# Optimization experiments

Hardware: AMD Instinct MI355X
Metric: run time of the kernel (lower is better)

The kernel has to match this reference:

```python
import jax, jax.numpy as jnp
import numpy as np

B, T, D, NH = 2, 2048, 2048, 16
HID = D  # hidden_dim must equal emb_dim for the source's fc2(x1) to type-check
HD = D // NH
EPS = 1e-5


def setup_inputs() -> dict:
    key = jax.random.key(0)
    ks = jax.random.split(key, 16)
    s = 0.02
    inp = {
        "x": jax.random.normal(ks[0], (B, T, D), jnp.float32),
        "Wq": jax.random.normal(ks[1], (D, D), jnp.float32) * s,
        "bq": jnp.zeros((D,), jnp.float32),
        "Wk": jax.random.normal(ks[2], (D, D), jnp.float32) * s,
        "bk": jnp.zeros((D,), jnp.float32),
        "Wv": jax.random.normal(ks[3], (D, D), jnp.float32) * s,
        "bv": jnp.zeros((D,), jnp.float32),
        "Wo": jax.random.normal(ks[4], (D, D), jnp.float32) * s,
        "bo": jnp.zeros((D,), jnp.float32),
        "scale1": jnp.ones((D,), jnp.float32),
        "scale2": jnp.ones((D,), jnp.float32),
        "W1": jax.random.normal(ks[5], (D, HID), jnp.float32) * s,
        "W2": jax.random.normal(ks[6], (D, HID), jnp.float32) * s,  # fc2: Linear(emb_dim, hidden_dim)
        "W3": jax.random.normal(ks[7], (HID, D), jnp.float32) * s,
    }
    return inp


def _rmsnorm(x, scale):
    m = jnp.mean(x * x, axis=-1, keepdims=True)
    return scale * (x * jax.lax.rsqrt(m + EPS))


def _attention(x, Wq, bq, Wk, bk, Wv, bv, Wo, bo):
    b, t, _ = x.shape
    q = (x @ Wq + bq).reshape(b, t, NH, HD)
    k = (x @ Wk + bk).reshape(b, t, NH, HD)
    v = (x @ Wv + bv).reshape(b, t, NH, HD)
    # energy: [B, H, T, T]; softmax over keys, scaled by 1/sqrt(head_dim); NO causal mask in source
    energy = jnp.einsum("bqhd,bkhd->bhqk", q, k) / jnp.sqrt(jnp.float32(HD))
    attn = jax.nn.softmax(energy, axis=-1)
    out = jnp.einsum("bhqk,bkhd->bqhd", attn, v).reshape(b, t, D)
    return out @ Wo + bo


def _ffn(x, W1, W2, W3):
    x1 = x @ W1                       # [B,T,HID]
    x2 = x1 @ W2                      # source quirk: fc2 applied to x1 (hidden_dim == emb_dim)
    return (x1 * jax.nn.sigmoid(x1) * x2) @ W3


def reference(x, Wq, bq, Wk, bk, Wv, bv, Wo, bo, scale1, scale2, W1, W2, W3):
    shortcut = x
    h = _rmsnorm(x, scale1)
    h = _attention(h, Wq, bq, Wk, bk, Wv, bv, Wo, bo)
    h = shortcut + h
    h = _rmsnorm(h, scale2)
    h = _ffn(h, W1, W2, W3)
    # source adds the ORIGINAL input again (shortcut never reassigned)
    return h + shortcut
```

## Files before the change

kernel.cpp:

```cpp
#include <hip/hip_runtime.h>

typedef __bf16 bf16x8 __attribute__((ext_vector_type(8)));
typedef __bf16 bf16x4v __attribute__((ext_vector_type(4)));
typedef float  f32x4  __attribute__((ext_vector_type(4)));

#define LDS_AS(p) ((__attribute__((address_space(3))) void*)(p))
#define GLB_AS(p) ((const __attribute__((address_space(1))) void*)(p))

#define QSCL (0.08838834764831845f * 1.4426950408889634f)

struct TP { const float* s[7]; __bf16* d[7]; float sc[7]; };
__global__ __launch_bounds__(256) void transpose_convert_all(TP p) {
  const float* __restrict__ W = p.s[blockIdx.z];
  __bf16* __restrict__ Wt = p.d[blockIdx.z];
  const float sc = p.sc[blockIdx.z];
  __shared__ float tile[32][33];
  const int tx = threadIdx.x & 31, ty = threadIdx.x >> 5;
  const int n0 = blockIdx.x * 32, k0 = blockIdx.y * 32;
#pragma unroll
  for (int j = 0; j < 4; ++j)
    tile[ty + j * 8][tx] = W[(size_t)(k0 + ty + j * 8) * 2048 + n0 + tx];
  __syncthreads();
#pragma unroll
  for (int j = 0; j < 4; ++j)
    Wt[(size_t)(n0 + ty + j * 8) * 2048 + k0 + tx] = (__bf16)(tile[tx][ty + j * 8] * sc);
}

__global__ __launch_bounds__(256) void rmsnorm_k(
    const float* __restrict__ x, const float* __restrict__ scale,
    __bf16* __restrict__ out) {
  const int row = blockIdx.x, t = threadIdx.x;
  const float4* xr = (const float4*)(x + (size_t)row * 2048);
  float4 a = xr[t], b2 = xr[t + 256];
  float ss = a.x * a.x + a.y * a.y + a.z * a.z + a.w * a.w +
             b2.x * b2.x + b2.y * b2.y + b2.z * b2.z + b2.w * b2.w;
#pragma unroll
  for (int ofs = 32; ofs; ofs >>= 1) ss += __shfl_xor(ss, ofs, 64);
  __shared__ float red[4];
  if ((t & 63) == 0) red[t >> 6] = ss;
  __syncthreads();
  ss = red[0] + red[1] + red[2] + red[3];
  const float rs = rsqrtf(ss * (1.f / 2048.f) + 1e-5f);
  const float4* sr = (const float4*)scale;
  float4 s1 = sr[t], s2 = sr[t + 256];
  __bf16* orow = out + (size_t)row * 2048;
  orow[t * 4 + 0] = (__bf16)(a.x * rs * s1.x);
  orow[t * 4 + 1] = (__bf16)(a.y * rs * s1.y);
  orow[t * 4 + 2] = (__bf16)(a.z * rs * s1.z);
  orow[t * 4 + 3] = (__bf16)(a.w * rs * s1.w);
  orow[(t + 256) * 4 + 0] = (__bf16)(b2.x * rs * s2.x);
  orow[(t + 256) * 4 + 1] = (__bf16)(b2.y * rs * s2.y);
  orow[(t + 256) * 4 + 2] = (__bf16)(b2.z * rs * s2.z);
  orow[(t + 256) * 4 + 3] = (__bf16)(b2.w * rs * s2.w);
}

template <bool OUTF32, bool HASBIAS, bool HASRES, bool SILU, bool VTRANS>
__global__ __launch_bounds__(512, 2) void gemm_bt2(
    const __bf16* __restrict__ A, const __bf16* __restrict__ Bt,
    const float* __restrict__ bias, const float* __restrict__ res,
    const __bf16* __restrict__ ew, void* __restrict__ Cout,
    int M, int N, int Kd) {
  __shared__ __attribute__((aligned(16))) char lds[2][3][16384];

  const int tid = threadIdx.x;
  const int w = tid >> 6, l = tid & 63;
  const int wr = w >> 1, wc = w & 1;
  const int lm = l & 15, lq = l >> 4;

  const int flat = blockIdx.y * 16 + blockIdx.x;
  const int swz = (flat & 7) * 32 + (flat >> 3);
  const int bx = swz >> 4, by = swz & 15;
  const int N0 = bx * 128, M0 = by * 256;

  const int srow = w * 8 + (l >> 3);
  const int scol = ((l & 7) ^ (l >> 3)) * 8;
  const __bf16* aS = A + (size_t)(M0 + srow) * Kd + scol;
  const __bf16* bS = Bt + (size_t)(N0 + srow) * Kd + scol;

  auto stageHT = [&](int t, int s, int db) {
    char* dst = lds[db][s] + w * 1024;
    const __bf16* src = (s == 0) ? (bS + t * 64)
                                 : (aS + (size_t)(s - 1) * 128 * Kd + t * 64);
    __builtin_amdgcn_global_load_lds(GLB_AS(src), LDS_AS(dst), 16, 0, 0);
    __builtin_amdgcn_global_load_lds(GLB_AS(src + (size_t)64 * Kd), LDS_AS(dst + 8192), 16, 0, 0);
  };

  f32x4 acc[4][4];
#pragma unroll
  for (int m = 0; m < 4; ++m)
#pragma unroll
    for (int n = 0; n < 4; ++n)
#pragma unroll
      for (int e = 0; e < 4; ++e) acc[m][n][e] = 0.f;

  const int swzr = (lm & 7) << 4;
  const int c0 = (lq * 16) ^ swzr;
  const int c1 = ((64 + lq * 16)) ^ swzr;
  const int arow = (wr & 1) * 8192 + lm * 128;
  const int brow = wc * 8192 + lm * 128;

  stageHT(0, 0, 0); stageHT(0, 1, 0); stageHT(0, 2, 0);
  stageHT(1, 0, 1); stageHT(1, 1, 1);
  asm volatile("s_waitcnt vmcnt(4)" ::: "memory");
  __builtin_amdgcn_s_barrier();

  const int NT = Kd >> 6;
  bf16x8 af[4][2], bfr[4][2];

#define BAR()                                            \
  do {                                                   \
    asm volatile("" ::: "memory");                       \
    __builtin_amdgcn_s_barrier();                        \
    asm volatile("" ::: "memory");                       \
  } while (0)

#define MFMA_QUAD(MB, NB)                                                          \
  do {                                                                             \
    _Pragma("unroll") for (int m = 0; m < 2; ++m)                                  \
      _Pragma("unroll") for (int n = 0; n < 2; ++n) {                              \
        acc[(MB) + m][(NB) + n] = __builtin_amdgcn_mfma_f32_16x16x32_bf16(         \
            af[(MB) + m][0], bfr[(NB) + n][0], acc[(MB) + m][(NB) + n], 0, 0, 0);  \
        acc[(MB) + m][(NB) + n] = __builtin_amdgcn_mfma_f32_16x16x32_bf16(         \
            af[(MB) + m][1], bfr[(NB) + n][1], acc[(MB) + m][(NB) + n], 0, 0, 0);  \
      }                                                                            \
  } while (0)

#define TILE_BODY(T, BUF)                                                       \
  do {                                                                          \
    const char* Ab = lds[BUF][1 + (wr >> 1)];                                   \
    const char* Bb = lds[BUF][0];                                               \
         \
    _Pragma("unroll") for (int m = 0; m < 4; ++m) {                             \
      af[m][0] = *(const bf16x8*)(Ab + arow + m * 2048 + c0);                   \
      af[m][1] = *(const bf16x8*)(Ab + arow + m * 2048 + c1);                   \
    }                                                                           \
    _Pragma("unroll") for (int n = 0; n < 4; ++n) {                             \
      bfr[n][0] = *(const bf16x8*)(Bb + brow + n * 2048 + c0);                  \
      bfr[n][1] = *(const bf16x8*)(Bb + brow + n * 2048 + c1);                  \
    }                                                                           \
    if ((T) + 1 < NT) stageHT((T) + 1, 2, (BUF) ^ 1);                           \
    BAR();                                                                      \
    __builtin_amdgcn_s_setprio(1);                                              \
    MFMA_QUAD(0, 0);                                                            \
    __builtin_amdgcn_s_setprio(0);                                              \
    asm volatile("s_waitcnt lgkmcnt(0)" ::: "memory");                          \
    BAR();                                                                      \
                                          \
    if ((T) + 2 < NT) stageHT((T) + 2, 0, BUF);                                 \
    BAR();                                                                      \
    __builtin_amdgcn_s_setprio(1);                                              \
    MFMA_QUAD(0, 2);                                                            \
    __builtin_amdgcn_s_setprio(0);                                              \
    BAR();                                                                      \
                                          \
    if ((T) + 2 < NT) stageHT((T) + 2, 1, BUF);                                 \
    BAR();                                                                      \
    __builtin_amdgcn_s_setprio(1);                                              \
    MFMA_QUAD(2, 0);                                                            \
    __builtin_amdgcn_s_setprio(0);                                              \
    BAR();                                                                      \
                                             \
    __builtin_amdgcn_s_setprio(1);                                              \
    MFMA_QUAD(2, 2);                                                            \
    __builtin_amdgcn_s_setprio(0);                                              \
    if ((T) + 2 < NT) { asm volatile("s_waitcnt vmcnt(4)" ::: "memory"); }      \
    else { asm volatile("s_waitcnt vmcnt(0)" ::: "memory"); }                   \
    BAR();                                                                      \
  } while (0)

  for (int tp = 0; tp < NT; tp += 2) {
    TILE_BODY(tp, 0);
    TILE_BODY(tp + 1, 1);
  }
#undef TILE_BODY
#undef MFMA_QUAD
#undef BAR

#pragma unroll
  for (int mt = 0; mt < 4; ++mt) {
#pragma unroll
    for (int nt = 0; nt < 4; ++nt) {
      const int col = N0 + wc * 64 + nt * 16 + lm;
      float bv = 0.f;
      if (HASBIAS) bv = bias[col];
      if (VTRANS) {
        const int rw0 = M0 + wr * 64 + mt * 16 + lq * 4;
        const int bidx = rw0 >> 11, tok = rw0 & 2047;
        bf16x4v pk;
#pragma unroll
        for (int i = 0; i < 4; ++i) pk[i] = (__bf16)(acc[mt][nt][i] + bv);
        *(bf16x4v*)((__bf16*)Cout + ((size_t)(bidx * 2048 + col)) * 2048 + tok) = pk;
      } else {
#pragma unroll
        for (int i = 0; i < 4; ++i) {
          const int row = M0 + wr * 64 + mt * 16 + lq * 4 + i;
          const size_t off = (size_t)row * N + col;
          float v = acc[mt][nt][i] + bv;
          if (HASRES) v += res[off];
          if (SILU) {
            const float x1v = (float)ew[off];
            v = x1v * (1.f / (1.f + __expf(-x1v))) * v;
          }
          if (OUTF32) ((float*)Cout)[off] = v;
          else ((__bf16*)Cout)[off] = (__bf16)v;
        }
      }
    }
  }
}

__global__ __launch_bounds__(512, 2) void gemm_qkv(
    const __bf16* __restrict__ A, const __bf16* __restrict__ Bt,
    const float* __restrict__ bq, const float* __restrict__ bk,
    __bf16* __restrict__ Qout, __bf16* __restrict__ Kout, int Kd) {
  __shared__ __attribute__((aligned(16))) char lds[2][4][16384];

  const int tid = threadIdx.x;
  const int w = tid >> 6, l = tid & 63;
  const int wr = w >> 2, wc = w & 3;
  const int lm = l & 15, lq = l >> 4;

  const int flat = blockIdx.y * 16 + blockIdx.x;
  const int swz = (flat & 7) * 32 + (flat >> 3);
  const int bx = swz >> 4, by = swz & 15;
  const int N0 = bx * 256, M0 = by * 256;

  const int srow = w * 8 + (l >> 3);
  const int scol = ((l & 7) ^ (l >> 3)) * 8;
  const __bf16* aS = A + (size_t)(M0 + srow) * Kd + scol;
  const __bf16* bS = Bt + (size_t)(N0 + srow) * Kd + scol;

  auto stageHT = [&](int t, int s, int db) {
    char* dst = lds[db][s] + w * 1024;
    const __bf16* src = (s >= 2) ? (aS + (size_t)(s - 2) * 128 * Kd + t * 64)
                                 : (bS + (size_t)s * 128 * Kd + t * 64);
    __builtin_amdgcn_global_load_lds(GLB_AS(src), LDS_AS(dst), 16, 0, 0);
    __builtin_amdgcn_global_load_lds(GLB_AS(src + (size_t)64 * Kd), LDS_AS(dst + 8192), 16, 0, 0);
  };

  f32x4 acc[8][4];
#pragma unroll
  for (int m = 0; m < 8; ++m)
#pragma unroll
    for (int n = 0; n < 4; ++n)
#pragma unroll
      for (int e = 0; e < 4; ++e) acc[m][n][e] = 0.f;

  const int swzr = (lm & 7) << 4;
  const int c0 = (lq * 16) ^ swzr;
  const int c1 = ((64 + lq * 16)) ^ swzr;
  const int arow = lm * 128;
  const int brow = ((wc & 1) * 64 + lm) * 128;

  stageHT(0, 0, 0); stageHT(0, 1, 0); stageHT(0, 2, 0); stageHT(0, 3, 0);
  stageHT(1, 0, 1); stageHT(1, 1, 1); stageHT(1, 2, 1);
  asm volatile("s_waitcnt vmcnt(6)" ::: "memory");
  __builtin_amdgcn_s_barrier();

  const int NT = Kd >> 6;
  bf16x8 af[4][2], bfr[4][2];

#define BAR()                                            \
  do {                                                   \
    asm volatile("" ::: "memory");                       \
    __builtin_amdgcn_s_barrier();                        \
    asm volatile("" ::: "memory");                       \
  } while (0)

#define MFMA_QUAD(MB, NB)                                                          \
  do {                                                                             \
    _Pragma("unroll") for (int m = 0; m < 4; ++m)                                  \
      _Pragma("unroll") for (int n = 0; n < 2; ++n) {                              \
        acc[(MB) + m][(NB) + n] = __builtin_amdgcn_mfma_f32_16x16x32_bf16(         \
            af[m][0], bfr[(NB) + n][0], acc[(MB) + m][(NB) + n], 0, 0, 0);         \
        acc[(MB) + m][(NB) + n] = __builtin_amdgcn_mfma_f32_16x16x32_bf16(         \
            af[m][1], bfr[(NB) + n][1], acc[(MB) + m][(NB) + n], 0, 0, 0);         \
      }                                                                            \
  } while (0)

#define TILE_BODY(T, BUF)                                                       \
  do {                                                                          \
    const char* Ab = lds[BUF][2 + wr];                                          \
    const char* Bb = lds[BUF][wc >> 1];                                         \
    _Pragma("unroll") for (int m = 0; m < 4; ++m) {                             \
      af[m][0] = *(const bf16x8*)(Ab + arow + m * 2048 + c0);                   \
      af[m][1] = *(const bf16x8*)(Ab + arow + m * 2048 + c1);                   \
    }                                                                           \
    _Pragma("unroll") for (int n = 0; n < 4; ++n) {                             \
      bfr[n][0] = *(const bf16x8*)(Bb + brow + n * 2048 + c0);                  \
      bfr[n][1] = *(const bf16x8*)(Bb + brow + n * 2048 + c1);                  \
    }                                                                           \
    if ((T) + 1 < NT) stageHT((T) + 1, 3, (BUF) ^ 1);                           \
    BAR();                                                                      \
    __builtin_amdgcn_s_setprio(1);                                              \
    MFMA_QUAD(0, 0);                                                            \
    __builtin_amdgcn_s_setprio(0);                                              \
    asm volatile("s_waitcnt lgkmcnt(0)" ::: "memory");                          \
    BAR();                                                                      \
    if ((T) + 2 < NT) stageHT((T) + 2, 0, BUF);                                 \
    BAR();                                                                      \
    __builtin_amdgcn_s_setprio(1);                                              \
    MFMA_QUAD(0, 2);                                                            \
    __builtin_amdgcn_s_setprio(0);                                              \
    BAR();                                                                      \
    _Pragma("unroll") for (int m = 0; m < 4; ++m) {                             \
      af[m][0] = *(const bf16x8*)(Ab + arow + (m + 4) * 2048 + c0);             \
      af[m][1] = *(const bf16x8*)(Ab + arow + (m + 4) * 2048 + c1);             \
    }                                                                           \
    if ((T) + 2 < NT) stageHT((T) + 2, 1, BUF);                                 \
    BAR();                                                                      \
    __builtin_amdgcn_s_setprio(1);                                              \
    MFMA_QUAD(4, 0);                                                            \
    __builtin_amdgcn_s_setprio(0);                                              \
    asm volatile("s_waitcnt lgkmcnt(0)" ::: "memory");                          \
    BAR();                                                                      \
    if ((T) + 2 < NT) stageHT((T) + 2, 2, BUF);                                 \
    BAR();                                                                      \
    __builtin_amdgcn_s_setprio(1);                                              \
    MFMA_QUAD(4, 2);                                                            \
    __builtin_amdgcn_s_setprio(0);                                              \
    if ((T) + 2 < NT) { asm volatile("s_waitcnt vmcnt(6)" ::: "memory"); }      \
    else { asm volatile("s_waitcnt vmcnt(0)" ::: "memory"); }                   \
    BAR();                                                                      \
  } while (0)

  for (int tp = 0; tp < NT; tp += 2) {
    TILE_BODY(tp, 0);
    TILE_BODY(tp + 1, 1);
  }
#undef TILE_BODY
#undef MFMA_QUAD
#undef BAR

  const int seg = N0 >> 11;
  const int nbase = N0 & 2047;
  const float* bb = (seg == 0) ? bq : bk;
  const float bsc = (seg == 0) ? QSCL : 1.f;
  __bf16* dst = (seg == 0) ? Qout : Kout;
#pragma unroll
  for (int m = 0; m < 8; ++m) {
#pragma unroll
    for (int n = 0; n < 4; ++n) {
      const int col = nbase + wc * 64 + n * 16 + lm;
      const float bvv = bb[col] * bsc;
#pragma unroll
      for (int i = 0; i < 4; ++i) {
        const int row = M0 + wr * 128 + m * 16 + lq * 4 + i;
        dst[(size_t)row * 2048 + col] = (__bf16)(acc[m][n][i] + bvv);
      }
    }
  }
}

__global__ __launch_bounds__(256, 2) void attn_mfma(
    const __bf16* __restrict__ Q, const __bf16* __restrict__ K,
    const __bf16* __restrict__ Vt, __bf16* __restrict__ O) {
  __shared__ __attribute__((aligned(16))) char KsL[2][16 * 1024];
  __shared__ __attribute__((aligned(16))) char VsL[2][16 * 1024];

  const int t = threadIdx.x;
  const int w = t >> 6, l = t & 63;
  const int lm = l & 15, quad = l >> 4;
  const int flat = (blockIdx.z * gridDim.y + blockIdx.y) * gridDim.x + blockIdx.x;
  const int swz = (flat & 7) * 64 + (flat >> 3);
  const int b = swz >> 8;
  const int h = (swz >> 4) & 15;
  const int q0 = (swz & 15) * 128;
  const size_t Ds = 2048;
  const size_t hoff = (size_t)h * 128;
  const size_t bbase = (size_t)b * 2048;
  const int slq = (lm << 2) | quad;
  const int sl16 = (slq ^ ((slq >> 3) & 7)) * 16;

  const int slog = l ^ ((l >> 3) & 7);
  const int krow = slog >> 2, kcol = (slog & 3) * 8;
  const int vth = l & 3, vd = l >> 2;

  bf16x8 onesv;
#pragma unroll
  for (int i = 0; i < 8; ++i) onesv[i] = (__bf16)1.0f;

  bf16x8 qf[2][4];
#pragma unroll
  for (int ntq = 0; ntq < 2; ++ntq)
#pragma unroll
    for (int ks = 0; ks < 4; ++ks)
      qf[ntq][ks] = *(const bf16x8*)(Q + (bbase + q0 + w * 32 + ntq * 16 + lm) * Ds + hoff + ks * 32 + quad * 8);

  f32x4 oacc[2][8];
#pragma unroll
  for (int ntq = 0; ntq < 2; ++ntq)
#pragma unroll
    for (int nv = 0; nv < 8; ++nv)
#pragma unroll
      for (int e = 0; e < 4; ++e) oacc[ntq][nv][e] = 0.f;
  f32x4 lacc[2];
#pragma unroll
  for (int ntq = 0; ntq < 2; ++ntq)
#pragma unroll
    for (int e = 0; e < 4; ++e) lacc[ntq][e] = 0.f;

  bf16x8 vreg[4];

  auto loadV = [&](int kt) {
#pragma unroll
    for (int i = 0; i < 4; ++i) {
      const int chunk = w * 4 + i;
      const int nv = chunk >> 1, c = chunk & 1;
      vreg[i] = *(const bf16x8*)(Vt + (bbase + hoff + nv * 16 + vd) * Ds + kt + c * 32 + vth * 8);
    }
  };
  auto stageK = [&](int kt, char* Kb) {
#pragma unroll
    for (int i = 0; i < 4; ++i) {
      const __bf16* src = K + (bbase + kt + i * 16 + krow) * Ds + hoff + w * 32 + kcol;
      __builtin_amdgcn_global_load_lds(GLB_AS(src), LDS_AS(Kb + (i * 4 + w) * 1024), 16, 0, 0);
    }
  };
  auto writeV = [&](char* Vb) {
    const int slot_a = (vd << 2) | ((vth & 1) << 1);
    const int o_a = (slot_a ^ ((vd >> 1) & 7)) * 16 + (vth >> 1) * 8;
#pragma unroll
    for (int i = 0; i < 4; ++i) {
      char* base = Vb + (w * 4 + i) * 1024;
      uint4 u = *(const uint4*)&vreg[i];
      *(uint2*)(base + o_a) = make_uint2(u.x, u.y);
      *(uint2*)(base + (o_a ^ 16)) = make_uint2(u.z, u.w);
    }
  };

  loadV(0);
  stageK(0, KsL[0]);
  writeV(VsL[0]);

  for (int it = 0; it < 32; ++it) {
    __syncthreads();
    const int cur = it & 1;
    const bool more = (it + 1) < 32;
    if (more) { loadV((it + 1) * 64); stageK((it + 1) * 64, KsL[(it + 1) & 1]); }

    const char* Kb = KsL[cur];
    const char* Vb = VsL[cur];

    f32x4 st[4][2];
#pragma unroll
    for (int mtk = 0; mtk < 4; ++mtk)
#pragma unroll
      for (int ntq = 0; ntq < 2; ++ntq)
#pragma unroll
        for (int e = 0; e < 4; ++e) st[mtk][ntq][e] = 0.f;
    __builtin_amdgcn_s_setprio(1);
#pragma unroll
    for (int ks = 0; ks < 4; ++ks) {
#pragma unroll
      for (int mtk = 0; mtk < 4; ++mtk) {
        bf16x8 kf = *(const bf16x8*)(Kb + (mtk * 4 + ks) * 1024 + sl16);
        st[mtk][0] = __builtin_amdgcn_mfma_f32_16x16x32_bf16(kf, qf[0][ks], st[mtk][0], 0, 0, 0);
        st[mtk][1] = __builtin_amdgcn_mfma_f32_16x16x32_bf16(kf, qf[1][ks], st[mtk][1], 0, 0, 0);
      }
    }
    __builtin_amdgcn_s_setprio(0);

#pragma unroll
    for (int c = 0; c < 2; ++c) {
      bf16x8 pf[2];
#pragma unroll
      for (int ntq = 0; ntq < 2; ++ntq) {
#pragma unroll
        for (int half = 0; half < 2; ++half) {
          const f32x4 sv = st[c * 2 + half][ntq];
#pragma unroll
          for (int r = 0; r < 4; ++r)
            pf[ntq][half * 4 + r] = (__bf16)exp2f(sv[r]);
        }
      }
      __builtin_amdgcn_s_setprio(1);
      lacc[0] = __builtin_amdgcn_mfma_f32_16x16x32_bf16(pf[0], onesv, lacc[0], 0, 0, 0);
      lacc[1] = __builtin_amdgcn_mfma_f32_16x16x32_bf16(pf[1], onesv, lacc[1], 0, 0, 0);
#pragma unroll
      for (int nv = 0; nv < 8; ++nv) {
        bf16x8 vf = *(const bf16x8*)(Vb + (nv * 2 + c) * 1024 + sl16);
        oacc[0][nv] = __builtin_amdgcn_mfma_f32_16x16x32_bf16(pf[0], vf, oacc[0][nv], 0, 0, 0);
        oacc[1][nv] = __builtin_amdgcn_mfma_f32_16x16x32_bf16(pf[1], vf, oacc[1][nv], 0, 0, 0);
      }
      __builtin_amdgcn_s_setprio(0);
    }

    if (more) writeV(VsL[(it + 1) & 1]);
  }

  float oinv[2][4];
#pragma unroll
  for (int ntq = 0; ntq < 2; ++ntq)
#pragma unroll
    for (int r = 0; r < 4; ++r)
      oinv[ntq][r] = 1.f / lacc[ntq][r];

#pragma unroll
  for (int ntq = 0; ntq < 2; ++ntq)
#pragma unroll
    for (int nv = 0; nv < 8; ++nv)
#pragma unroll
      for (int r = 0; r < 4; ++r) {
        const int qrow = q0 + w * 32 + ntq * 16 + quad * 4 + r;
        O[(bbase + qrow) * Ds + hoff + nv * 16 + lm] = (__bf16)(oacc[ntq][nv][r] * oinv[ntq][r]);
      }
}

extern "C" void kernel_launch(void* const* d_in, const int* in_sizes, int n_in,
                              void* d_out, int out_size, void* d_ws, size_t ws_size,
                              hipStream_t stream) {
  const float* x      = (const float*)d_in[0];
  const float* Wq     = (const float*)d_in[1];
  const float* bq     = (const float*)d_in[2];
  const float* Wk     = (const float*)d_in[3];
  const float* bk     = (const float*)d_in[4];
  const float* Wv     = (const float*)d_in[5];
  const float* bv     = (const float*)d_in[6];
  const float* Wo     = (const float*)d_in[7];
  const float* bo     = (const float*)d_in[8];
  const float* scale1 = (const float*)d_in[9];
  const float* scale2 = (const float*)d_in[10];
  const float* W1     = (const float*)d_in[11];
  const float* W2     = (const float*)d_in[12];
  const float* W3     = (const float*)d_in[13];

  const int M = 4096, N = 2048, Kd = 2048;
  char* ws = (char*)d_ws;
  const size_t WT_B = (size_t)2048 * 2048 * 2;
  const size_t ACT_B = (size_t)4096 * 2048 * 2;
  __bf16* wt[7];
  size_t off = 0;
  for (int i = 0; i < 7; ++i) { wt[i] = (__bf16*)(ws + off); off += WT_B; }
  __bf16* hn1  = (__bf16*)(ws + off); off += ACT_B;
  __bf16* Qb   = (__bf16*)(ws + off); off += ACT_B;
  __bf16* Kb   = (__bf16*)(ws + off); off += ACT_B;
  __bf16* VtG  = (__bf16*)(ws + off); off += ACT_B;
  __bf16* attn = (__bf16*)(ws + off); off += ACT_B;
  __bf16* hn2  = (__bf16*)(ws + off); off += ACT_B;
  __bf16* x1b  = (__bf16*)(ws + off); off += ACT_B;
  __bf16* fmb  = (__bf16*)(ws + off); off += ACT_B;

  dim3 tb(256);
  {
    TP p;
    p.s[0] = Wq; p.s[1] = Wk; p.s[2] = Wv; p.s[3] = Wo; p.s[4] = W1; p.s[5] = W2; p.s[6] = W3;
    for (int i = 0; i < 7; ++i) { p.d[i] = wt[i]; p.sc[i] = 1.f; }
    p.sc[0] = QSCL;
    transpose_convert_all<<<dim3(64, 64, 7), tb, 0, stream>>>(p);
  }

  rmsnorm_k<<<4096, tb, 0, stream>>>(x, scale1, hn1);

  gemm_qkv<<<dim3(16, 16), dim3(512), 0, stream>>>(hn1, wt[0], bq, bk, Qb, Kb, Kd);
  gemm_bt2<false, true, false, false, true><<<dim3(16, 16), dim3(512), 0, stream>>>(
      hn1, wt[2], bv, nullptr, nullptr, VtG, M, 2048, Kd);

  dim3 ag(2048 / 128, 16, 2);
  attn_mfma<<<ag, tb, 0, stream>>>(Qb, Kb, VtG, attn);

  dim3 gg2(16, 16);
  gemm_bt2<true, true, true, false, false><<<gg2, dim3(512), 0, stream>>>(
      attn, wt[3], bo, x, nullptr, d_out, M, N, Kd);

  rmsnorm_k<<<4096, tb, 0, stream>>>((const float*)d_out, scale2, hn2);

  gemm_bt2<false, false, false, false, false><<<gg2, dim3(512), 0, stream>>>(
      hn2, wt[4], nullptr, nullptr, nullptr, x1b, M, N, Kd);
  gemm_bt2<false, false, false, true, false><<<gg2, dim3(512), 0, stream>>>(
      x1b, wt[5], nullptr, nullptr, x1b, fmb, M, N, Kd);
  gemm_bt2<true, false, true, false, false><<<gg2, dim3(512), 0, stream>>>(
      fmb, wt[6], nullptr, x, nullptr, d_out, M, N, Kd);
}
```

Measured before the change: 561.0 us.

## Split attention block across eight waves with sixteen query rows each

The attention kernel now launches 512 threads per block instead of 256, and each wave handles 16 query rows instead of 32. K staging and V loading are redistributed so eight waves share the same 128-row tile loads. This cuts per-wave register use (fewer accumulators and score tiles), which should allow higher occupancy and better latency hiding. In exchange, each wave does half as much MFMA work per K/V LDS read, so LDS fragment reuse drops and more waves contend at barriers.

```diff
diff --git a/kernel.cpp b/kernel.cpp
--- a/kernel.cpp
+++ b/kernel.cpp
@@ -129,7 +129,6 @@
   do {                                                                          \
     const char* Ab = lds[BUF][1 + (wr >> 1)];                                   \
     const char* Bb = lds[BUF][0];                                               \
-         \
     _Pragma("unroll") for (int m = 0; m < 4; ++m) {                             \
       af[m][0] = *(const bf16x8*)(Ab + arow + m * 2048 + c0);                   \
       af[m][1] = *(const bf16x8*)(Ab + arow + m * 2048 + c1);                   \
@@ -145,21 +144,18 @@
     __builtin_amdgcn_s_setprio(0);                                              \
     asm volatile("s_waitcnt lgkmcnt(0)" ::: "memory");                          \
     BAR();                                                                      \
-                                          \
     if ((T) + 2 < NT) stageHT((T) + 2, 0, BUF);                                 \
     BAR();                                                                      \
     __builtin_amdgcn_s_setprio(1);                                              \
     MFMA_QUAD(0, 2);                                                            \
     __builtin_amdgcn_s_setprio(0);                                              \
     BAR();                                                                      \
-                                          \
     if ((T) + 2 < NT) stageHT((T) + 2, 1, BUF);                                 \
     BAR();                                                                      \
     __builtin_amdgcn_s_setprio(1);                                              \
     MFMA_QUAD(2, 0);                                                            \
     __builtin_amdgcn_s_setprio(0);                                              \
     BAR();                                                                      \
-                                             \
     __builtin_amdgcn_s_setprio(1);                                              \
     MFMA_QUAD(2, 2);                                                            \
     __builtin_amdgcn_s_setprio(0);                                              \
@@ -352,7 +348,7 @@
   }
 }
 
-__global__ __launch_bounds__(256, 2) void attn_mfma(
+__global__ __launch_bounds__(512, 4) void attn_mfma(
     const __bf16* __restrict__ Q, const __bf16* __restrict__ K,
     const __bf16* __restrict__ Vt, __bf16* __restrict__ O) {
   __shared__ __attribute__((aligned(16))) char KsL[2][16 * 1024];
@@ -380,49 +376,45 @@
 #pragma unroll
   for (int i = 0; i < 8; ++i) onesv[i] = (__bf16)1.0f;
 
-  bf16x8 qf[2][4];
-#pragma unroll
-  for (int ntq = 0; ntq < 2; ++ntq)
-#pragma unroll
-    for (int ks = 0; ks < 4; ++ks)
-      qf[ntq][ks] = *(const bf16x8*)(Q + (bbase + q0 + w * 32 + ntq * 16 + lm) * Ds + hoff + ks * 32 + quad * 8);
-
-  f32x4 oacc[2][8];
-#pragma unroll
-  for (int ntq = 0; ntq < 2; ++ntq)
-#pragma unroll
-    for (int nv = 0; nv < 8; ++nv)
-#pragma unroll
-      for (int e = 0; e < 4; ++e) oacc[ntq][nv][e] = 0.f;
-  f32x4 lacc[2];
-#pragma unroll
-  for (int ntq = 0; ntq < 2; ++ntq)
-#pragma unroll
-    for (int e = 0; e < 4; ++e) lacc[ntq][e] = 0.f;
-
-  bf16x8 vreg[4];
+  bf16x8 qf[4];
+#pragma unroll
+  for (int ks = 0; ks < 4; ++ks)
+    qf[ks] = *(const bf16x8*)(Q + (bbase + q0 + w * 16 + lm) * Ds + hoff + ks * 32 + quad * 8);
+
+  f32x4 oacc[8];
+#pragma unroll
+  for (int nv = 0; nv < 8; ++nv)
+#pragma unroll
+    for (int e = 0; e < 4; ++e) oacc[nv][e] = 0.f;
+  f32x4 lacc;
+#pragma unroll
+  for (int e = 0; e < 4; ++e) lacc[e] = 0.f;
+
+  bf16x8 vreg[2];
 
   auto loadV = [&](int kt) {
 #pragma unroll
-    for (int i = 0; i < 4; ++i) {
-      const int chunk = w * 4 + i;
+    for (int i = 0; i < 2; ++i) {
+      const int chunk = w * 2 + i;
       const int nv = chunk >> 1, c = chunk & 1;
       vreg[i] = *(const bf16x8*)(Vt + (bbase + hoff + nv * 16 + vd) * Ds + kt + c * 32 + vth * 8);
     }
   };
   auto stageK = [&](int kt, char* Kb) {
 #pragma unroll
-    for (int i = 0; i < 4; ++i) {
-      const __bf16* src = K + (bbase + kt + i * 16 + krow) * Ds + hoff + w * 32 + kcol;
-      __builtin_amdgcn_global_load_lds(GLB_AS(src), LDS_AS(Kb + (i * 4 + w) * 1024), 16, 0, 0);
+    for (int i = 0; i < 2; ++i) {
+      const int chunk = i * 8 + w;
+      const int mtk = chunk >> 2, ks2 = chunk & 3;
+      const __bf16* src = K + (bbase + kt + mtk * 16 + krow) * Ds + hoff + ks2 * 32 + kcol;
+      __builtin_amdgcn_global_load_lds(GLB_AS(src), LDS_AS(Kb + chunk * 1024), 16, 0, 0);
     }
   };
   auto writeV = [&](char* Vb) {
     const int slot_a = (vd << 2) | ((vth & 1) << 1);
     const int o_a = (slot_a ^ ((vd >> 1) & 7)) * 16 + (vth >> 1) * 8;
 #pragma unroll
-    for (int i = 0; i < 4; ++i) {
-      char* base = Vb + (w * 4 + i) * 1024;
+    for (int i = 0; i < 2; ++i) {
+      char* base = Vb + (w * 2 + i) * 1024;
       uint4 u = *(const uint4*)&vreg[i];
       *(uint2*)(base + o_a) = make_uint2(u.x, u.y);
       *(uint2*)(base + (o_a ^ 16)) = make_uint2(u.z, u.w);
@@ -442,46 +434,38 @@
     const char* Kb = KsL[cur];
     const char* Vb = VsL[cur];
 
-    f32x4 st[4][2];
+    f32x4 st[4];
 #pragma unroll
     for (int mtk = 0; mtk < 4; ++mtk)
 #pragma unroll
-      for (int ntq = 0; ntq < 2; ++ntq)
-#pragma unroll
-        for (int e = 0; e < 4; ++e) st[mtk][ntq][e] = 0.f;
+      for (int e = 0; e < 4; ++e) st[mtk][e] = 0.f;
     __builtin_amdgcn_s_setprio(1);
 #pragma unroll
     for (int ks = 0; ks < 4; ++ks) {
 #pragma unroll
       for (int mtk = 0; mtk < 4; ++mtk) {
         bf16x8 kf = *(const bf16x8*)(Kb + (mtk * 4 + ks) * 1024 + sl16);
-        st[mtk][0] = __builtin_amdgcn_mfma_f32_16x16x32_bf16(kf, qf[0][ks], st[mtk][0], 0, 0, 0);
-        st[mtk][1] = __builtin_amdgcn_mfma_f32_16x16x32_bf16(kf, qf[1][ks], st[mtk][1], 0, 0, 0);
+        st[mtk] = __builtin_amdgcn_mfma_f32_16x16x32_bf16(kf, qf[ks], st[mtk], 0, 0, 0);
       }
     }
     __builtin_amdgcn_s_setprio(0);
 
 #pragma unroll
     for (int c = 0; c < 2; ++c) {
-      bf16x8 pf[2];
-#pragma unroll
-      for (int ntq = 0; ntq < 2; ++ntq) {
-#pragma unroll
-        for (int half = 0; half < 2; ++half) {
-          const f32x4 sv = st[c * 2 + half][ntq];
-#pragma unroll
-          for (int r = 0; r < 4; ++r)
-            pf[ntq][half * 4 + r] = (__bf16)exp2f(sv[r]);
-        }
+      bf16x8 pf;
+#pragma unroll
+      for (int half = 0; half < 2; ++half) {
+        const f32x4 sv = st[c * 2 + half];
+#pragma unroll
+        for (int r = 0; r < 4; ++r)
+          pf[half * 4 + r] = (__bf16)exp2f(sv[r]);
       }
       __builtin_amdgcn_s_setprio(1);
-      lacc[0] = __builtin_amdgcn_mfma_f32_16x16x32_bf16(pf[0], onesv, lacc[0], 0, 0, 0);
-      lacc[1] = __builtin_amdgcn_mfma_f32_16x16x32_bf16(pf[1], onesv, lacc[1], 0, 0, 0);
+      lacc = __builtin_amdgcn_mfma_f32_16x16x32_bf16(pf, onesv, lacc, 0, 0, 0);
 #pragma unroll
       for (int nv = 0; nv < 8; ++nv) {
         bf16x8 vf = *(const bf16x8*)(Vb + (nv * 2 + c) * 1024 + sl16);
-        oacc[0][nv] = __builtin_amdgcn_mfma_f32_16x16x32_bf16(pf[0], vf, oacc[0][nv], 0, 0, 0);
-        oacc[1][nv] = __builtin_amdgcn_mfma_f32_16x16x32_bf16(pf[1], vf, oacc[1][nv], 0, 0, 0);
+        oacc[nv] = __builtin_amdgcn_mfma_f32_16x16x32_bf16(pf, vf, oacc[nv], 0, 0, 0);
       }
       __builtin_amdgcn_s_setprio(0);
     }
@@ -489,22 +473,18 @@
     if (more) writeV(VsL[(it + 1) & 1]);
   }
 
-  float oinv[2][4];
-#pragma unroll
-  for (int ntq = 0; ntq < 2; ++ntq)
-#pragma unroll
-    for (int r = 0; r < 4; ++r)
-      oinv[ntq][r] = 1.f / lacc[ntq][r];
-
-#pragma unroll
-  for (int ntq = 0; ntq < 2; ++ntq)
-#pragma unroll
-    for (int nv = 0; nv < 8; ++nv)
-#pragma unroll
-      for (int r = 0; r < 4; ++r) {
-        const int qrow = q0 + w * 32 + ntq * 16 + quad * 4 + r;
-        O[(bbase + qrow) * Ds + hoff + nv * 16 + lm] = (__bf16)(oacc[ntq][nv][r] * oinv[ntq][r]);
-      }
+  float oinv[4];
+#pragma unroll
+  for (int r = 0; r < 4; ++r)
+    oinv[r] = 1.f / lacc[r];
+
+#pragma unroll
+  for (int nv = 0; nv < 8; ++nv)
+#pragma unroll
+    for (int r = 0; r < 4; ++r) {
+      const int qrow = q0 + w * 16 + quad * 4 + r;
+      O[(bbase + qrow) * Ds + hoff + nv * 16 + lm] = (__bf16)(oacc[nv][r] * oinv[r]);
+    }
 }
 
 extern "C" void kernel_launch(void* const* d_in, const int* in_sizes, int n_in,
@@ -557,7 +537,7 @@
       hn1, wt[2], bv, nullptr, nullptr, VtG, M, 2048, Kd);
 
   dim3 ag(2048 / 128, 16, 2);
-  attn_mfma<<<ag, tb, 0, stream>>>(Qb, Kb, VtG, attn);
+  attn_mfma<<<ag, dim3(512), 0, stream>>>(Qb, Kb, VtG, attn);
 
   dim3 gg2(16, 16);
   gemm_bt2<true, true, true, false, false><<<gg2, dim3(512), 0, stream>>>(
```

After: 561.4 us. No clear change (+0.1%).
